# Performance work log

Measured on AMD Instinct MI355X. Metric: run time of the kernel, lower is better.

Reference implementation:

```python
import jax, jax.numpy as jnp
import numpy as np

NUM_USERS = 1_000_000
NUM_ITEMS = 1_000_000
EMB_DIM = 64
HIDDEN = 128
BATCH = 16384


def setup_inputs() -> dict:
    key = jax.random.key(0)
    ks = jax.random.split(key, 8)
    users = jax.random.randint(ks[0], (BATCH,), 0, NUM_USERS)
    items = jax.random.randint(ks[1], (BATCH,), 0, NUM_ITEMS)
    user_emb = 0.01 * jax.random.normal(ks[2], (NUM_USERS, EMB_DIM), dtype=jnp.float32)
    item_emb = 0.01 * jax.random.normal(ks[3], (NUM_ITEMS, EMB_DIM), dtype=jnp.float32)
    user_bias = jnp.zeros((NUM_USERS, 1), dtype=jnp.float32)
    item_bias = jnp.zeros((NUM_ITEMS, 1), dtype=jnp.float32)
    global_bias = jnp.zeros((1,), dtype=jnp.float32)
    # xavier_uniform for Linear layers
    lim1 = float(np.sqrt(6.0 / (2 * EMB_DIM + HIDDEN)))
    w1 = jax.random.uniform(ks[4], (HIDDEN, 2 * EMB_DIM), minval=-lim1, maxval=lim1, dtype=jnp.float32)
    b1 = jnp.zeros((HIDDEN,), dtype=jnp.float32)
    lim2 = float(np.sqrt(6.0 / (HIDDEN + 1)))
    w2 = jax.random.uniform(ks[5], (1, HIDDEN), minval=-lim2, maxval=lim2, dtype=jnp.float32)
    b2 = jnp.zeros((1,), dtype=jnp.float32)
    return {
        "users": users, "items": items,
        "user_emb": user_emb, "item_emb": item_emb,
        "user_bias": user_bias, "item_bias": item_bias,
        "global_bias": global_bias,
        "w1": w1, "b1": b1, "w2": w2, "b2": b2,
    }


def reference(users, items, user_emb, item_emb, user_bias, item_bias,
              global_bias, w1, b1, w2, b2):
    user_vecs = user_emb[users]            # [B, D]
    item_vecs = item_emb[items]            # [B, D]
    dot = jnp.sum(user_vecs * item_vecs, axis=1)  # [B]
    mlp_in = jnp.concatenate([user_vecs, item_vecs], axis=1)  # [B, 2D]
    h = jax.nn.relu(mlp_in @ w1.T + b1)    # [B, H]
    mlp_score = (h @ w2.T + b2)[:, 0]      # [B]
    scores = (dot
              + user_bias[users][:, 0]
              + item_bias[items][:, 0]
              + global_bias
              + mlp_score)
    return scores
```

## Files before the change

### kernel.cpp

```cpp
#include <hip/hip_runtime.h>

#define BLOCK 256
#define EPB 64
#define LDK 136

typedef __attribute__((ext_vector_type(8))) short short8;
typedef __attribute__((ext_vector_type(4))) float f32x4;

__device__ __forceinline__ unsigned short f2bf(float f) {
    unsigned u = __float_as_uint(f);
    u += 0x7FFF + ((u >> 16) & 1);
    return (unsigned short)(u >> 16);
}

__global__ __launch_bounds__(BLOCK) void mf_fused(
    const int* __restrict__ users, const int* __restrict__ items,
    const float* __restrict__ user_emb, const float* __restrict__ item_emb,
    const float* __restrict__ user_bias, const float* __restrict__ item_bias,
    const float* __restrict__ global_bias,
    const float* __restrict__ w1, const float* __restrict__ b1,
    const float* __restrict__ w2, const float* __restrict__ b2,
    float* __restrict__ out)
{
    __shared__ unsigned short sA[EPB * LDK];
    __shared__ unsigned short sB[128 * LDK];
    __shared__ float sSum[EPB];
    __shared__ float sB1[128];
    __shared__ float sW2[128];

    const int tid = threadIdx.x;
    const int e0 = blockIdx.x * EPB;

    {
        const int c = tid & 31;
        const int h0 = tid >> 5;
        #pragma unroll
        for (int it = 0; it < 16; ++it) {
            const int h = h0 + it * 8;
            const float4 wv = *(const float4*)(w1 + h * 128 + c * 4);
            ushort4 pk;
            pk.x = f2bf(wv.x); pk.y = f2bf(wv.y); pk.z = f2bf(wv.z); pk.w = f2bf(wv.w);
            *(ushort4*)&sB[h * LDK + c * 4] = pk;
        }
    }
    if (tid < 128) { sB1[tid] = b1[tid]; sW2[tid] = w2[tid]; }

    {
        const int c = tid & 15;
        const int er = tid >> 4;
        int uid[4], iid[4];
        #pragma unroll
        for (int it = 0; it < 4; ++it) {
            uid[it] = users[e0 + er + it * 16];
            iid[it] = items[e0 + er + it * 16];
        }
        float4 u4[4], v4[4];
        #pragma unroll
        for (int it = 0; it < 4; ++it) {
            u4[it] = *(const float4*)(user_emb + (size_t)uid[it] * 64 + c * 4);
            v4[it] = *(const float4*)(item_emb + (size_t)iid[it] * 64 + c * 4);
        }
        const float gb = global_bias[0] + b2[0];
        #pragma unroll
        for (int it = 0; it < 4; ++it) {
            const int eloc = er + it * 16;
            ushort4 pu, pv;
            pu.x = f2bf(u4[it].x); pu.y = f2bf(u4[it].y);
            pu.z = f2bf(u4[it].z); pu.w = f2bf(u4[it].w);
            pv.x = f2bf(v4[it].x); pv.y = f2bf(v4[it].y);
            pv.z = f2bf(v4[it].z); pv.w = f2bf(v4[it].w);
            *(ushort4*)&sA[eloc * LDK + c * 4]      = pu;
            *(ushort4*)&sA[eloc * LDK + 64 + c * 4] = pv;
            float p = u4[it].x * v4[it].x + u4[it].y * v4[it].y
                    + u4[it].z * v4[it].z + u4[it].w * v4[it].w;
            p += __shfl_xor(p, 1);
            p += __shfl_xor(p, 2);
            p += __shfl_xor(p, 4);
            p += __shfl_xor(p, 8);
            if (c == 0)
                sSum[eloc] = p + user_bias[uid[it]] + item_bias[iid[it]] + gb;
        }
    }

    __syncthreads();

    const int lane = tid & 63;
    const int wv   = tid >> 6;
    const int quad = lane >> 4;
    const int nidx = lane & 15;
    const int eRow = wv * 16;

    f32x4 acc[8];
    #pragma unroll
    for (int nt = 0; nt < 8; ++nt) acc[nt] = (f32x4){0.f, 0.f, 0.f, 0.f};

    #pragma unroll
    for (int kk = 0; kk < 4; ++kk) {
        const short8 a = *(const short8*)&sA[(eRow + nidx) * LDK + kk * 32 + quad * 8];
        #pragma unroll
        for (int nt = 0; nt < 8; ++nt) {
            const short8 b = *(const short8*)&sB[(nt * 16 + nidx) * LDK + kk * 32 + quad * 8];
            acc[nt] = __builtin_amdgcn_mfma_f32_16x16x32_bf16(a, b, acc[nt], 0, 0, 0);
        }
    }

    float p0 = 0.f, p1 = 0.f, p2 = 0.f, p3 = 0.f;
    #pragma unroll
    for (int nt = 0; nt < 8; ++nt) {
        const int h = nt * 16 + nidx;
        const float b1v = sB1[h];
        const float w2v = sW2[h];
        p0 += fmaxf(acc[nt][0] + b1v, 0.f) * w2v;
        p1 += fmaxf(acc[nt][1] + b1v, 0.f) * w2v;
        p2 += fmaxf(acc[nt][2] + b1v, 0.f) * w2v;
        p3 += fmaxf(acc[nt][3] + b1v, 0.f) * w2v;
    }
    #define RED16(p) { p += __shfl_xor(p, 1); p += __shfl_xor(p, 2); \
                       p += __shfl_xor(p, 4); p += __shfl_xor(p, 8); }
    RED16(p0) RED16(p1) RED16(p2) RED16(p3)

    if (nidx == 0) {
        const int eb = eRow + quad * 4;
        float4 o;
        o.x = p0 + sSum[eb + 0];
        o.y = p1 + sSum[eb + 1];
        o.z = p2 + sSum[eb + 2];
        o.w = p3 + sSum[eb + 3];
        *(float4*)(out + e0 + eb) = o;
    }
}

extern "C" void kernel_launch(void* const* d_in, const int* in_sizes, int n_in,
                              void* d_out, int out_size, void* d_ws, size_t ws_size,
                              hipStream_t stream) {
    const int*   users       = (const int*)d_in[0];
    const int*   items       = (const int*)d_in[1];
    const float* user_emb    = (const float*)d_in[2];
    const float* item_emb    = (const float*)d_in[3];
    const float* user_bias   = (const float*)d_in[4];
    const float* item_bias   = (const float*)d_in[5];
    const float* global_bias = (const float*)d_in[6];
    const float* w1          = (const float*)d_in[7];
    const float* b1          = (const float*)d_in[8];
    const float* w2          = (const float*)d_in[9];
    const float* b2          = (const float*)d_in[10];
    float* out = (float*)d_out;

    const int batch = in_sizes[0];
    const int grid = batch / EPB;
    mf_fused<<<grid, BLOCK, 0, stream>>>(users, items, user_emb, item_emb,
        user_bias, item_bias, global_bias, w1, b1, w2, b2, out);
}
```

Measured before the change: 403.4 us.

## Halve elements per block and split MLP hidden dimension across waves

Each block now handles 32 elements instead of 64, doubling the grid. The four waves split the work as two row tiles times two hidden halves, and the partial MLP scores are combined through shared memory after an extra barrier. Index loads are hoisted ahead of the weight conversion so gathers can be issued earlier. The intent is more blocks in flight to hide gather latency, at the cost of converting w1 to bf16 twice as often overall.

```diff
diff --git a/kernel.cpp b/kernel.cpp
--- a/kernel.cpp
+++ b/kernel.cpp
@@ -1,7 +1,7 @@
 #include <hip/hip_runtime.h>
 
 #define BLOCK 256
-#define EPB 64
+#define EPB 32
 #define LDK 136
 
 typedef __attribute__((ext_vector_type(8))) short short8;
@@ -13,7 +13,7 @@
     return (unsigned short)(u >> 16);
 }
 
-__global__ __launch_bounds__(BLOCK) void mf_fused(
+__global__ __launch_bounds__(BLOCK, 2) void mf_fused(
     const int* __restrict__ users, const int* __restrict__ items,
     const float* __restrict__ user_emb, const float* __restrict__ item_emb,
     const float* __restrict__ user_bias, const float* __restrict__ item_bias,
@@ -25,89 +25,93 @@
     __shared__ unsigned short sA[EPB * LDK];
     __shared__ unsigned short sB[128 * LDK];
     __shared__ float sSum[EPB];
+    __shared__ float sP[2][EPB];
     __shared__ float sB1[128];
     __shared__ float sW2[128];
 
     const int tid = threadIdx.x;
     const int e0 = blockIdx.x * EPB;
 
+    const int c  = tid & 15;
+    const int er = tid >> 4;
+    const int uid_a = users[e0 + er];
+    const int uid_b = users[e0 + er + 16];
+    const int iid_a = items[e0 + er];
+    const int iid_b = items[e0 + er + 16];
+
+    if (tid < 128) { sB1[tid] = b1[tid]; sW2[tid] = w2[tid]; }
+
     {
-        const int c = tid & 31;
+        const int c2 = tid & 31;
         const int h0 = tid >> 5;
         #pragma unroll
         for (int it = 0; it < 16; ++it) {
             const int h = h0 + it * 8;
-            const float4 wv = *(const float4*)(w1 + h * 128 + c * 4);
+            const float4 wv = *(const float4*)(w1 + h * 128 + c2 * 4);
             ushort4 pk;
             pk.x = f2bf(wv.x); pk.y = f2bf(wv.y); pk.z = f2bf(wv.z); pk.w = f2bf(wv.w);
-            *(ushort4*)&sB[h * LDK + c * 4] = pk;
+            *(ushort4*)&sB[h * LDK + c2 * 4] = pk;
         }
     }
-    if (tid < 128) { sB1[tid] = b1[tid]; sW2[tid] = w2[tid]; }
 
     {
-        const int c = tid & 15;
-        const int er = tid >> 4;
-        int uid[4], iid[4];
-        #pragma unroll
-        for (int it = 0; it < 4; ++it) {
-            uid[it] = users[e0 + er + it * 16];
-            iid[it] = items[e0 + er + it * 16];
-        }
-        float4 u4[4], v4[4];
-        #pragma unroll
-        for (int it = 0; it < 4; ++it) {
-            u4[it] = *(const float4*)(user_emb + (size_t)uid[it] * 64 + c * 4);
-            v4[it] = *(const float4*)(item_emb + (size_t)iid[it] * 64 + c * 4);
-        }
+        const float4 ua = *(const float4*)(user_emb + (size_t)uid_a * 64 + c * 4);
+        const float4 va = *(const float4*)(item_emb + (size_t)iid_a * 64 + c * 4);
+        const float4 ub = *(const float4*)(user_emb + (size_t)uid_b * 64 + c * 4);
+        const float4 vb = *(const float4*)(item_emb + (size_t)iid_b * 64 + c * 4);
         const float gb = global_bias[0] + b2[0];
-        #pragma unroll
-        for (int it = 0; it < 4; ++it) {
-            const int eloc = er + it * 16;
-            ushort4 pu, pv;
-            pu.x = f2bf(u4[it].x); pu.y = f2bf(u4[it].y);
-            pu.z = f2bf(u4[it].z); pu.w = f2bf(u4[it].w);
-            pv.x = f2bf(v4[it].x); pv.y = f2bf(v4[it].y);
-            pv.z = f2bf(v4[it].z); pv.w = f2bf(v4[it].w);
-            *(ushort4*)&sA[eloc * LDK + c * 4]      = pu;
-            *(ushort4*)&sA[eloc * LDK + 64 + c * 4] = pv;
-            float p = u4[it].x * v4[it].x + u4[it].y * v4[it].y
-                    + u4[it].z * v4[it].z + u4[it].w * v4[it].w;
-            p += __shfl_xor(p, 1);
-            p += __shfl_xor(p, 2);
-            p += __shfl_xor(p, 4);
-            p += __shfl_xor(p, 8);
-            if (c == 0)
-                sSum[eloc] = p + user_bias[uid[it]] + item_bias[iid[it]] + gb;
+        const float uba = user_bias[uid_a], ubb = user_bias[uid_b];
+        const float iba = item_bias[iid_a], ibb = item_bias[iid_b];
+
+        ushort4 pk;
+        pk.x = f2bf(ua.x); pk.y = f2bf(ua.y); pk.z = f2bf(ua.z); pk.w = f2bf(ua.w);
+        *(ushort4*)&sA[er * LDK + c * 4] = pk;
+        pk.x = f2bf(va.x); pk.y = f2bf(va.y); pk.z = f2bf(va.z); pk.w = f2bf(va.w);
+        *(ushort4*)&sA[er * LDK + 64 + c * 4] = pk;
+        pk.x = f2bf(ub.x); pk.y = f2bf(ub.y); pk.z = f2bf(ub.z); pk.w = f2bf(ub.w);
+        *(ushort4*)&sA[(er + 16) * LDK + c * 4] = pk;
+        pk.x = f2bf(vb.x); pk.y = f2bf(vb.y); pk.z = f2bf(vb.z); pk.w = f2bf(vb.w);
+        *(ushort4*)&sA[(er + 16) * LDK + 64 + c * 4] = pk;
+
+        float pa = ua.x * va.x + ua.y * va.y + ua.z * va.z + ua.w * va.w;
+        float pb = ub.x * vb.x + ub.y * vb.y + ub.z * vb.z + ub.w * vb.w;
+        #define RED16(p) { p += __shfl_xor(p, 1); p += __shfl_xor(p, 2); \
+                           p += __shfl_xor(p, 4); p += __shfl_xor(p, 8); }
+        RED16(pa) RED16(pb)
+        if (c == 0) {
+            sSum[er]      = pa + uba + iba + gb;
+            sSum[er + 16] = pb + ubb + ibb + gb;
         }
     }
 
     __syncthreads();
 
-    const int lane = tid & 63;
-    const int wv   = tid >> 6;
-    const int quad = lane >> 4;
-    const int nidx = lane & 15;
-    const int eRow = wv * 16;
+    const int lane  = tid & 63;
+    const int wv    = tid >> 6;
+    const int quad  = lane >> 4;
+    const int nidx  = lane & 15;
+    const int mrow0 = (wv & 1) * 16;
+    const int nhalf = wv >> 1;
+    const int hbase = nhalf * 64;
 
-    f32x4 acc[8];
+    f32x4 acc[4];
     #pragma unroll
-    for (int nt = 0; nt < 8; ++nt) acc[nt] = (f32x4){0.f, 0.f, 0.f, 0.f};
+    for (int nt = 0; nt < 4; ++nt) acc[nt] = (f32x4){0.f, 0.f, 0.f, 0.f};
 
     #pragma unroll
     for (int kk = 0; kk < 4; ++kk) {
-        const short8 a = *(const short8*)&sA[(eRow + nidx) * LDK + kk * 32 + quad * 8];
+        const short8 a = *(const short8*)&sA[(mrow0 + nidx) * LDK + kk * 32 + quad * 8];
         #pragma unroll
-        for (int nt = 0; nt < 8; ++nt) {
-            const short8 b = *(const short8*)&sB[(nt * 16 + nidx) * LDK + kk * 32 + quad * 8];
+        for (int nt = 0; nt < 4; ++nt) {
+            const short8 b = *(const short8*)&sB[(hbase + nt * 16 + nidx) * LDK + kk * 32 + quad * 8];
             acc[nt] = __builtin_amdgcn_mfma_f32_16x16x32_bf16(a, b, acc[nt], 0, 0, 0);
         }
     }
 
     float p0 = 0.f, p1 = 0.f, p2 = 0.f, p3 = 0.f;
     #pragma unroll
-    for (int nt = 0; nt < 8; ++nt) {
-        const int h = nt * 16 + nidx;
+    for (int nt = 0; nt < 4; ++nt) {
+        const int h = hbase + nt * 16 + nidx;
         const float b1v = sB1[h];
         const float w2v = sW2[h];
         p0 += fmaxf(acc[nt][0] + b1v, 0.f) * w2v;
@@ -115,19 +119,19 @@
         p2 += fmaxf(acc[nt][2] + b1v, 0.f) * w2v;
         p3 += fmaxf(acc[nt][3] + b1v, 0.f) * w2v;
     }
-    #define RED16(p) { p += __shfl_xor(p, 1); p += __shfl_xor(p, 2); \
-                       p += __shfl_xor(p, 4); p += __shfl_xor(p, 8); }
     RED16(p0) RED16(p1) RED16(p2) RED16(p3)
 
     if (nidx == 0) {
-        const int eb = eRow + quad * 4;
-        float4 o;
-        o.x = p0 + sSum[eb + 0];
-        o.y = p1 + sSum[eb + 1];
-        o.z = p2 + sSum[eb + 2];
-        o.w = p3 + sSum[eb + 3];
-        *(float4*)(out + e0 + eb) = o;
+        const int eb = mrow0 + quad * 4;
+        sP[nhalf][eb + 0] = p0;
+        sP[nhalf][eb + 1] = p1;
+        sP[nhalf][eb + 2] = p2;
+        sP[nhalf][eb + 3] = p3;
     }
+    __syncthreads();
+
+    if (tid < EPB)
+        out[e0 + tid] = sSum[tid] + sP[0][tid] + sP[1][tid];
 }
 
 extern "C" void kernel_launch(void* const* d_in, const int* in_sizes, int n_in,
```

Result: no change. 400.7 us (-0.7%).
